# Kernel tuning notes

Hardware: AMD Instinct MI355X
Metric: run time of the kernel (lower is better)

Reference implementation:

```python
import jax, jax.numpy as jnp
import numpy as np

ALPHA = 0.2  # LeakyReLU negative slope
NEG_INF = -9e15


def setup_inputs() -> dict:
    key = jax.random.key(0)
    k1, k2, k3, k4 = jax.random.split(key, 4)
    B, N, Fin, Fout = 8, 2048, 512, 256
    x = jax.random.normal(k1, (B, N, Fin), dtype=jnp.float32)
    adj = jax.random.randint(k2, (B, N, N), 0, 2, dtype=jnp.int32)
    # xavier_uniform-like init, gain=1.414
    limW = 1.414 * np.sqrt(6.0 / (Fin + Fout))
    W = jax.random.uniform(k3, (Fin, Fout), jnp.float32, -limW, limW)
    lima = 1.414 * np.sqrt(6.0 / (2 * Fout + 1))
    a = jax.random.uniform(k4, (2 * Fout, 1), jnp.float32, -lima, lima)
    return {"x": x, "adj": adj, "W": W, "a": a}


def reference(x, adj, W, a):
    # x: [B,N,Fin], adj: [B,N,N], W: [Fin,Fout], a: [2*Fout,1]
    Fout = W.shape[1]
    h = jnp.einsum('bnf,fo->bno', x, W)                      # [B,N,Fout]
    a1 = a[:Fout, 0]                                         # source part
    a2 = a[Fout:, 0]                                         # target part
    # e_ij = LeakyReLU(a1.h_i + a2.h_j) -- decomposed, no O(N^2*2F) tensor
    s = h @ a1                                               # [B,N]
    t = h @ a2                                               # [B,N]
    e = jax.nn.leaky_relu(s[:, :, None] + t[:, None, :], ALPHA)  # [B,N,N]
    e = jnp.where(adj > 0, e, NEG_INF)
    attention = jax.nn.softmax(e, axis=2)                    # dropout p=0 (eval)
    h_prime = jnp.einsum('bij,bjo->bio', attention, h)       # [B,N,Fout]
    return jax.nn.elu(h_prime)                               # concat=True -> ELU
```

## Files before the change

kernel.cpp:

```cpp
#include <hip/hip_runtime.h>
#include <hip/hip_bf16.h>

typedef __attribute__((ext_vector_type(8))) short short8;
typedef __attribute__((ext_vector_type(4))) short short4v;
typedef __attribute__((ext_vector_type(4))) float f32x4;

constexpr int Bb = 8, NN = 2048, FIN = 512, FOUT = 256;
#define LRALPHA 0.2f
#define MFMA16(a, b, c) __builtin_amdgcn_mfma_f32_16x16x32_bf16((a), (b), (c), 0, 0, 0)

static __device__ __forceinline__ ushort f2bf(float f) {
    unsigned u = __float_as_uint(f);
    u += 0x7fffu + ((u >> 16) & 1u);
    return (ushort)(u >> 16);
}
static __device__ __forceinline__ float bf2f(ushort b) { return __uint_as_float(((unsigned)b) << 16); }

#define LDSBAR() do { asm volatile("s_waitcnt lgkmcnt(0)" ::: "memory"); \
                      __builtin_amdgcn_s_barrier(); \
                      asm volatile("" ::: "memory"); } while (0)
#define BARONLY() do { asm volatile("" ::: "memory"); \
                       __builtin_amdgcn_s_barrier(); \
                       asm volatile("" ::: "memory"); } while (0)

__global__ __launch_bounds__(256) void prep(const float* __restrict__ W,
                                            const float* __restrict__ a,
                                            ushort* __restrict__ WTh,
                                            ushort* __restrict__ WTl,
                                            float* __restrict__ wa1,
                                            float* __restrict__ wa2) {
    __shared__ float r1[4], r2[4];
    const int k = blockIdx.x, n = threadIdx.x;
    const int lane = n & 63, wv = n >> 6;
    const float w = W[(size_t)k * FOUT + n];
    const ushort hi = f2bf(w);
    WTh[(size_t)n * FIN + k] = hi;
    WTl[(size_t)n * FIN + k] = f2bf(w - bf2f(hi));
    float p1 = w * a[n], p2 = w * a[FOUT + n];
#pragma unroll
    for (int m = 1; m < 64; m <<= 1) {
        p1 += __shfl_xor(p1, m);
        p2 += __shfl_xor(p2, m);
    }
    if (lane == 0) { r1[wv] = p1; r2[wv] = p2; }
    __syncthreads();
    if (n == 0) {
        wa1[k] = r1[0] + r1[1] + r1[2] + r1[3];
        wa2[k] = r2[0] + r2[1] + r2[2] + r2[3];
    }
}

__global__ __launch_bounds__(512, 4) void gemm_h(const float* __restrict__ x,
                                                 const ushort* __restrict__ WTh,
                                                 const ushort* __restrict__ WTl,
                                                 const float* __restrict__ wa1,
                                                 const float* __restrict__ wa2,
                                                 ushort* __restrict__ hTh,
                                                 float* __restrict__ sv,
                                                 float* __restrict__ tv) {
    __shared__ ushort Ah[4][2][512];
    __shared__ ushort Tr[8][16][72];

    const int t = threadIdx.x, lane = t & 63, w = t >> 6;
    const int m0 = (blockIdx.x >> 1) * 64;
    const int n0 = (blockIdx.x & 1) * 128;

    const int lr = t >> 3, c8 = (t & 7) * 8;
    const int aif = lr >> 4, akstep = c8 >> 5, ak8 = (c8 >> 3) & 3;
    ushort* adst = &Ah[aif][akstep][(((ak8 << 4) | (lr & 15))) * 8];
    const float* xp = x + (size_t)(m0 + lr) * FIN + c8;

    const size_t boff = (size_t)(n0 + w * 16 + (lane & 15)) * FIN + (lane >> 4) * 8;
    const ushort* bph = WTh + boff;
    const ushort* bpl = WTl + boff;

    f32x4 acc[4];
#pragma unroll
    for (int f = 0; f < 4; ++f) acc[f] = (f32x4){0.f, 0.f, 0.f, 0.f};
    float sp = 0.f, tp = 0.f;

    float4 xa0 = *(const float4*)(xp + 0),  xa1 = *(const float4*)(xp + 4);
    float4 xb0 = *(const float4*)(xp + 64), xb1 = *(const float4*)(xp + 68);
    float4 xc0, xc1, xd0, xd1;
    short8 bhA0 = *(const short8*)(bph + 0),  blA0 = *(const short8*)(bpl + 0);
    short8 bhA1 = *(const short8*)(bph + 32), blA1 = *(const short8*)(bpl + 32);
    short8 bhB0, blB0, bhB1, blB1;

    auto phase = [&](int kt, const float4& c0, const float4& c1, float4& nx0, float4& nx1,
                     const short8& cbh0, const short8& cbl0, const short8& cbh1, const short8& cbl1,
                     short8& nbh0, short8& nbl0, short8& nbh1, short8& nbl1) {
        const int k0 = kt * 64;
        const float fv[8] = {c0.x, c0.y, c0.z, c0.w, c1.x, c1.y, c1.z, c1.w};
        short8 vh;
#pragma unroll
        for (int e = 0; e < 8; ++e) vh[e] = (short)f2bf(fv[e]);
        const float4 w1a = *(const float4*)(wa1 + k0 + c8);
        const float4 w1b = *(const float4*)(wa1 + k0 + c8 + 4);
        const float4 w2a = *(const float4*)(wa2 + k0 + c8);
        const float4 w2b = *(const float4*)(wa2 + k0 + c8 + 4);
        sp += fv[0]*w1a.x + fv[1]*w1a.y + fv[2]*w1a.z + fv[3]*w1a.w
            + fv[4]*w1b.x + fv[5]*w1b.y + fv[6]*w1b.z + fv[7]*w1b.w;
        tp += fv[0]*w2a.x + fv[1]*w2a.y + fv[2]*w2a.z + fv[3]*w2a.w
            + fv[4]*w2b.x + fv[5]*w2b.y + fv[6]*w2b.z + fv[7]*w2b.w;
        BARONLY();
        *(short8*)adst = vh;
        LDSBAR();
        const int kx = (kt + 2 < 8 ? kt + 2 : 7) * 64;
        nx0 = *(const float4*)(xp + kx);
        nx1 = *(const float4*)(xp + kx + 4);
        const int kb = (kt + 1 < 8 ? kt + 1 : 7) * 64;
        nbh0 = *(const short8*)(bph + kb);
        nbl0 = *(const short8*)(bpl + kb);
        nbh1 = *(const short8*)(bph + kb + 32);
        nbl1 = *(const short8*)(bpl + kb + 32);
#pragma unroll
        for (int f = 0; f < 4; ++f) {
            const short8 a0 = *(const short8*)&Ah[f][0][lane * 8];
            const short8 a1 = *(const short8*)&Ah[f][1][lane * 8];
            acc[f] = MFMA16(a0, cbh0, acc[f]);
            acc[f] = MFMA16(a0, cbl0, acc[f]);
            acc[f] = MFMA16(a1, cbh1, acc[f]);
            acc[f] = MFMA16(a1, cbl1, acc[f]);
        }
    };

    for (int kt = 0; kt < 8; kt += 4) {
        phase(kt + 0, xa0, xa1, xc0, xc1, bhA0, blA0, bhA1, blA1, bhB0, blB0, bhB1, blB1);
        phase(kt + 1, xb0, xb1, xd0, xd1, bhB0, blB0, bhB1, blB1, bhA0, blA0, bhA1, blA1);
        phase(kt + 2, xc0, xc1, xa0, xa1, bhA0, blA0, bhA1, blA1, bhB0, blB0, bhB1, blB1);
        phase(kt + 3, xd0, xd1, xb0, xb1, bhB0, blB0, bhB1, blB1, bhA0, blA0, bhA1, blA1);
    }

    sp += __shfl_xor(sp, 1, 8); sp += __shfl_xor(sp, 2, 8); sp += __shfl_xor(sp, 4, 8);
    tp += __shfl_xor(tp, 1, 8); tp += __shfl_xor(tp, 2, 8); tp += __shfl_xor(tp, 4, 8);
    if ((t & 7) == 0 && n0 == 0) {
        sv[m0 + lr] = sp;
        tv[m0 + lr] = tp;
    }

    const int rb = (lane >> 4) * 4;
#pragma unroll
    for (int f = 0; f < 4; ++f)
#pragma unroll
        for (int r = 0; r < 4; ++r)
            Tr[w][lane & 15][f * 16 + rb + r] = f2bf(acc[f][r]);
    __syncthreads();
    const int c = lane >> 2, rowb = (lane & 3) * 16;
    const ushort* src = &Tr[w][c][rowb];
    const short8 v0 = *(const short8*)src;
    const short8 v1 = *(const short8*)(src + 8);
    ushort* dst = hTh + ((size_t)(m0 >> 11) * FOUT + n0 + w * 16 + c) * NN + (m0 & 2047) + rowb;
    *(short8*)dst = v0;
    *(short8*)(dst + 8) = v1;
}

__global__ __launch_bounds__(512, 2) void gat_fused(const int* __restrict__ adj,
                                                    const ushort* __restrict__ hTh,
                                                    const float* __restrict__ sv,
                                                    const float* __restrict__ tv,
                                                    float* __restrict__ out) {
    __shared__ float t_l[NN];
    __shared__ ushort Pf[2][4][2][512];
    __shared__ float den_l[64];

    const int t = threadIdx.x, lane = t & 63, w = t >> 6;
    const int b = blockIdx.x & 7, i0 = (blockIdx.x >> 3) * 64;

    *(float4*)&t_l[t * 4] = *(const float4*)&tv[b * NN + t * 4];

    const int r = t >> 3, jn = (t & 7) * 8;
    const float s_i = sv[b * NN + i0 + r];
    const int* adjp = adj + ((size_t)b * NN + i0 + r) * NN + jn;
    const int pif = r >> 4, pkstep = jn >> 5, pk8 = (jn >> 3) & 3;
    ushort* pdst0 = &Pf[0][pif][pkstep][((pk8 << 4) | (r & 15)) * 8];
    ushort* pdst1 = &Pf[1][pif][pkstep][((pk8 << 4) | (r & 15)) * 8];

    const ushort* hb = hTh + (size_t)b * FOUT * NN;
    const ushort* h00 = hb + (size_t)(2 * w * 16 + (lane & 15)) * NN + (lane >> 4) * 8;
    const ushort* h10 = hb + (size_t)((2 * w + 1) * 16 + (lane & 15)) * NN + (lane >> 4) * 8;

    f32x4 acc[4][2];
#pragma unroll
    for (int f = 0; f < 4; ++f) {
        acc[f][0] = (f32x4){0.f, 0.f, 0.f, 0.f};
        acc[f][1] = (f32x4){0.f, 0.f, 0.f, 0.f};
    }
    float den_part = 0.f;

    int4 ajA0 = *(const int4*)(adjp),      ajA1 = *(const int4*)(adjp + 4);
    int4 ajB0 = *(const int4*)(adjp + 64), ajB1 = *(const int4*)(adjp + 68);
    int4 ajC0, ajC1, ajD0, ajD1;
    short8 X00 = *(const short8*)h00, X01 = *(const short8*)(h00 + 32);
    short8 X10 = *(const short8*)h10, X11 = *(const short8*)(h10 + 32);
    short8 Y00, Y01, Y10, Y11;

    __syncthreads();

    auto phase = [&](int jt, ushort* pdst, int rbuf,
                     const int4& ac0, const int4& ac1, int4& an0, int4& an1,
                     const short8& c00, const short8& c01, const short8& c10, const short8& c11,
                     short8& n00, short8& n01, short8& n10, short8& n11) {
        const int j0 = jt * 64;
        const int jH = min(j0 + 64, NN - 64);
        const int jA = min(j0 + 128, NN - 64);
        n00 = *(const short8*)(h00 + jH);
        n01 = *(const short8*)(h00 + jH + 32);
        n10 = *(const short8*)(h10 + jH);
        n11 = *(const short8*)(h10 + jH + 32);
        an0 = *(const int4*)(adjp + jA);
        an1 = *(const int4*)(adjp + jA + 4);
        const float4 tq0 = *(const float4*)&t_l[j0 + jn];
        const float4 tq1 = *(const float4*)&t_l[j0 + jn + 4];
        const float tvv[8] = {tq0.x, tq0.y, tq0.z, tq0.w, tq1.x, tq1.y, tq1.z, tq1.w};
        const int avs[8] = {ac0.x, ac0.y, ac0.z, ac0.w, ac1.x, ac1.y, ac1.z, ac1.w};
        short8 pv;
#pragma unroll
        for (int e = 0; e < 8; ++e) {
            float v = s_i + tvv[e];
            v = v > 0.f ? v : LRALPHA * v;
            const float wv = avs[e] > 0 ? __expf(v) : 0.f;
            const ushort hbv = f2bf(wv);
            den_part += bf2f(hbv);
            pv[e] = (short)hbv;
        }
        *(short8*)pdst = pv;
        LDSBAR();
        const ushort* pr = &Pf[rbuf][0][0][0] + lane * 8;
        __builtin_amdgcn_s_setprio(1);
#pragma unroll
        for (int f = 0; f < 4; ++f) {
            const short8 a0 = *(const short8*)(pr + f * 1024);
            const short8 a1 = *(const short8*)(pr + f * 1024 + 512);
            acc[f][0] = MFMA16(a0, c00, acc[f][0]);
            acc[f][0] = MFMA16(a1, c01, acc[f][0]);
            acc[f][1] = MFMA16(a0, c10, acc[f][1]);
            acc[f][1] = MFMA16(a1, c11, acc[f][1]);
        }
        __builtin_amdgcn_s_setprio(0);
    };

    for (int tt = 0; tt < NN / 64; tt += 4) {
        phase(tt + 0, pdst0, 0, ajA0, ajA1, ajC0, ajC1, X00, X01, X10, X11, Y00, Y01, Y10, Y11);
        phase(tt + 1, pdst1, 1, ajB0, ajB1, ajD0, ajD1, Y00, Y01, Y10, Y11, X00, X01, X10, X11);
        phase(tt + 2, pdst0, 0, ajC0, ajC1, ajA0, ajA1, X00, X01, X10, X11, Y00, Y01, Y10, Y11);
        phase(tt + 3, pdst1, 1, ajD0, ajD1, ajB0, ajB1, Y00, Y01, Y10, Y11, X00, X01, X10, X11);
    }

    den_part += __shfl_xor(den_part, 1, 8);
    den_part += __shfl_xor(den_part, 2, 8);
    den_part += __shfl_xor(den_part, 4, 8);
    if ((t & 7) == 0) den_l[r] = den_part;
    __syncthreads();

    const int rb = (lane >> 4) * 4;
#pragma unroll
    for (int f = 0; f < 4; ++f) {
#pragma unroll
        for (int rr = 0; rr < 4; ++rr) {
            const int row = f * 16 + rb + rr;
            const float inv = 1.0f / den_l[row];
#pragma unroll
            for (int cf = 0; cf < 2; ++cf) {
                float v = acc[f][cf][rr] * inv;
                v = v > 0.f ? v : expm1f(v);
                out[((size_t)b * NN + i0 + row) * FOUT + w * 32 + cf * 16 + (lane & 15)] = v;
            }
        }
    }
}

extern "C" void kernel_launch(void* const* d_in, const int* in_sizes, int n_in,
                              void* d_out, int out_size, void* d_ws, size_t ws_size,
                              hipStream_t stream) {
    const float* x   = (const float*)d_in[0];
    const int*   adj = (const int*)d_in[1];
    const float* W   = (const float*)d_in[2];
    const float* a   = (const float*)d_in[3];
    float* out = (float*)d_out;

    ushort* hTh = (ushort*)d_ws;
    float*  sv  = (float*)(hTh + (size_t)Bb * FOUT * NN);
    float*  tv  = sv + Bb * NN;
    ushort* WTh = (ushort*)(tv + Bb * NN);
    ushort* WTl = WTh + (size_t)FIN * FOUT;
    float*  wa1 = (float*)(WTl + (size_t)FIN * FOUT);
    float*  wa2 = wa1 + FIN;

    prep<<<FIN, 256, 0, stream>>>(W, a, WTh, WTl, wa1, wa2);
    gemm_h<<<512, 512, 0, stream>>>(x, WTh, WTl, wa1, wa2, hTh, sv, tv);
    gat_fused<<<256, 512, 0, stream>>>(adj, hTh, sv, tv, out);
}
```

Measured before the change: 270.5 us.

## Widen gemm_h tile to full output width and deepen adj prefetch in gat_fused

gemm_h now has each block compute all 256 output columns for 64 rows, with each wave owning two 16-column slices. This halves the grid and removes the duplicated x loads, bf16 conversion and s/t dot products that the two column-half blocks used to repeat, at the cost of more registers and lower occupancy. In gat_fused, adjacency loads are now issued four tiles ahead instead of two, and h loads are moved to after the MFMAs, to hide global latency for the int32 adj stream.

```diff
diff --git a/kernel.cpp b/kernel.cpp
--- a/kernel.cpp
+++ b/kernel.cpp
@@ -2,7 +2,6 @@
 #include <hip/hip_bf16.h>
 
 typedef __attribute__((ext_vector_type(8))) short short8;
-typedef __attribute__((ext_vector_type(4))) short short4v;
 typedef __attribute__((ext_vector_type(4))) float f32x4;
 
 constexpr int Bb = 8, NN = 2048, FIN = 512, FOUT = 256;
@@ -50,7 +49,7 @@
     }
 }
 
-__global__ __launch_bounds__(512, 4) void gemm_h(const float* __restrict__ x,
+__global__ __launch_bounds__(512, 2) void gemm_h(const float* __restrict__ x,
                                                  const ushort* __restrict__ WTh,
                                                  const ushort* __restrict__ WTl,
                                                  const float* __restrict__ wa1,
@@ -62,33 +61,40 @@
     __shared__ ushort Tr[8][16][72];
 
     const int t = threadIdx.x, lane = t & 63, w = t >> 6;
-    const int m0 = (blockIdx.x >> 1) * 64;
-    const int n0 = (blockIdx.x & 1) * 128;
+    const int m0 = blockIdx.x * 64;
 
     const int lr = t >> 3, c8 = (t & 7) * 8;
     const int aif = lr >> 4, akstep = c8 >> 5, ak8 = (c8 >> 3) & 3;
     ushort* adst = &Ah[aif][akstep][(((ak8 << 4) | (lr & 15))) * 8];
     const float* xp = x + (size_t)(m0 + lr) * FIN + c8;
 
-    const size_t boff = (size_t)(n0 + w * 16 + (lane & 15)) * FIN + (lane >> 4) * 8;
-    const ushort* bph = WTh + boff;
-    const ushort* bpl = WTl + boff;
-
-    f32x4 acc[4];
-#pragma unroll
-    for (int f = 0; f < 4; ++f) acc[f] = (f32x4){0.f, 0.f, 0.f, 0.f};
+    const size_t b0 = (size_t)(w * 32 + (lane & 15)) * FIN + (lane >> 4) * 8;
+    const size_t b1 = b0 + (size_t)16 * FIN;
+    const ushort *ph0 = WTh + b0, *pl0 = WTl + b0;
+    const ushort *ph1 = WTh + b1, *pl1 = WTl + b1;
+
+    f32x4 acc[4][2];
+#pragma unroll
+    for (int f = 0; f < 4; ++f) {
+        acc[f][0] = (f32x4){0.f, 0.f, 0.f, 0.f};
+        acc[f][1] = (f32x4){0.f, 0.f, 0.f, 0.f};
+    }
     float sp = 0.f, tp = 0.f;
 
     float4 xa0 = *(const float4*)(xp + 0),  xa1 = *(const float4*)(xp + 4);
     float4 xb0 = *(const float4*)(xp + 64), xb1 = *(const float4*)(xp + 68);
     float4 xc0, xc1, xd0, xd1;
-    short8 bhA0 = *(const short8*)(bph + 0),  blA0 = *(const short8*)(bpl + 0);
-    short8 bhA1 = *(const short8*)(bph + 32), blA1 = *(const short8*)(bpl + 32);
-    short8 bhB0, blB0, bhB1, blB1;
+    short8 A00 = *(const short8*)(ph0 + 0),  A01 = *(const short8*)(pl0 + 0);
+    short8 A02 = *(const short8*)(ph0 + 32), A03 = *(const short8*)(pl0 + 32);
+    short8 A10 = *(const short8*)(ph1 + 0),  A11 = *(const short8*)(pl1 + 0);
+    short8 A12 = *(const short8*)(ph1 + 32), A13 = *(const short8*)(pl1 + 32);
+    short8 B00, B01, B02, B03, B10, B11, B12, B13;
 
     auto phase = [&](int kt, const float4& c0, const float4& c1, float4& nx0, float4& nx1,
-                     const short8& cbh0, const short8& cbl0, const short8& cbh1, const short8& cbl1,
-                     short8& nbh0, short8& nbl0, short8& nbh1, short8& nbl1) {
+                     const short8& g00, const short8& g01, const short8& g02, const short8& g03,
+                     const short8& g10, const short8& g11, const short8& g12, const short8& g13,
+                     short8& n00, short8& n01, short8& n02, short8& n03,
+                     short8& n10, short8& n11, short8& n12, short8& n13) {
         const int k0 = kt * 64;
         const float fv[8] = {c0.x, c0.y, c0.z, c0.w, c1.x, c1.y, c1.z, c1.w};
         short8 vh;
@@ -109,49 +115,62 @@
         nx0 = *(const float4*)(xp + kx);
         nx1 = *(const float4*)(xp + kx + 4);
         const int kb = (kt + 1 < 8 ? kt + 1 : 7) * 64;
-        nbh0 = *(const short8*)(bph + kb);
-        nbl0 = *(const short8*)(bpl + kb);
-        nbh1 = *(const short8*)(bph + kb + 32);
-        nbl1 = *(const short8*)(bpl + kb + 32);
+        n00 = *(const short8*)(ph0 + kb);      n01 = *(const short8*)(pl0 + kb);
+        n02 = *(const short8*)(ph0 + kb + 32); n03 = *(const short8*)(pl0 + kb + 32);
+        n10 = *(const short8*)(ph1 + kb);      n11 = *(const short8*)(pl1 + kb);
+        n12 = *(const short8*)(ph1 + kb + 32); n13 = *(const short8*)(pl1 + kb + 32);
 #pragma unroll
         for (int f = 0; f < 4; ++f) {
             const short8 a0 = *(const short8*)&Ah[f][0][lane * 8];
             const short8 a1 = *(const short8*)&Ah[f][1][lane * 8];
-            acc[f] = MFMA16(a0, cbh0, acc[f]);
-            acc[f] = MFMA16(a0, cbl0, acc[f]);
-            acc[f] = MFMA16(a1, cbh1, acc[f]);
-            acc[f] = MFMA16(a1, cbl1, acc[f]);
+            acc[f][0] = MFMA16(a0, g00, acc[f][0]);
+            acc[f][0] = MFMA16(a0, g01, acc[f][0]);
+            acc[f][0] = MFMA16(a1, g02, acc[f][0]);
+            acc[f][0] = MFMA16(a1, g03, acc[f][0]);
+            acc[f][1] = MFMA16(a0, g10, acc[f][1]);
+            acc[f][1] = MFMA16(a0, g11, acc[f][1]);
+            acc[f][1] = MFMA16(a1, g12, acc[f][1]);
+            acc[f][1] = MFMA16(a1, g13, acc[f][1]);
         }
     };
 
     for (int kt = 0; kt < 8; kt += 4) {
-        phase(kt + 0, xa0, xa1, xc0, xc1, bhA0, blA0, bhA1, blA1, bhB0, blB0, bhB1, blB1);
-        phase(kt + 1, xb0, xb1, xd0, xd1, bhB0, blB0, bhB1, blB1, bhA0, blA0, bhA1, blA1);
-        phase(kt + 2, xc0, xc1, xa0, xa1, bhA0, blA0, bhA1, blA1, bhB0, blB0, bhB1, blB1);
-        phase(kt + 3, xd0, xd1, xb0, xb1, bhB0, blB0, bhB1, blB1, bhA0, blA0, bhA1, blA1);
+        phase(kt + 0, xa0, xa1, xc0, xc1, A00,A01,A02,A03,A10,A11,A12,A13,
+                                           B00,B01,B02,B03,B10,B11,B12,B13);
+        phase(kt + 1, xb0, xb1, xd0, xd1, B00,B01,B02,B03,B10,B11,B12,B13,
+                                           A00,A01,A02,A03,A10,A11,A12,A13);
+        phase(kt + 2, xc0, xc1, xa0, xa1, A00,A01,A02,A03,A10,A11,A12,A13,
+                                           B00,B01,B02,B03,B10,B11,B12,B13);
+        phase(kt + 3, xd0, xd1, xb0, xb1, B00,B01,B02,B03,B10,B11,B12,B13,
+                                           A00,A01,A02,A03,A10,A11,A12,A13);
     }
 
     sp += __shfl_xor(sp, 1, 8); sp += __shfl_xor(sp, 2, 8); sp += __shfl_xor(sp, 4, 8);
     tp += __shfl_xor(tp, 1, 8); tp += __shfl_xor(tp, 2, 8); tp += __shfl_xor(tp, 4, 8);
-    if ((t & 7) == 0 && n0 == 0) {
+    if ((t & 7) == 0) {
         sv[m0 + lr] = sp;
         tv[m0 + lr] = tp;
     }
 
     const int rb = (lane >> 4) * 4;
-#pragma unroll
-    for (int f = 0; f < 4; ++f)
-#pragma unroll
-        for (int r = 0; r < 4; ++r)
-            Tr[w][lane & 15][f * 16 + rb + r] = f2bf(acc[f][r]);
-    __syncthreads();
     const int c = lane >> 2, rowb = (lane & 3) * 16;
-    const ushort* src = &Tr[w][c][rowb];
-    const short8 v0 = *(const short8*)src;
-    const short8 v1 = *(const short8*)(src + 8);
-    ushort* dst = hTh + ((size_t)(m0 >> 11) * FOUT + n0 + w * 16 + c) * NN + (m0 & 2047) + rowb;
-    *(short8*)dst = v0;
-    *(short8*)(dst + 8) = v1;
+#pragma unroll
+    for (int p = 0; p < 2; ++p) {
+        __syncthreads();
+#pragma unroll
+        for (int f = 0; f < 4; ++f)
+#pragma unroll
+            for (int r = 0; r < 4; ++r)
+                Tr[w][lane & 15][f * 16 + rb + r] = f2bf(acc[f][p][r]);
+        __syncthreads();
+        const ushort* src = &Tr[w][c][rowb];
+        const short8 v0 = *(const short8*)src;
+        const short8 v1 = *(const short8*)(src + 8);
+        ushort* dst = hTh + ((size_t)(m0 >> 11) * FOUT + w * 32 + p * 16 + c) * NN
+                      + (m0 & 2047) + rowb;
+        *(short8*)dst = v0;
+        *(short8*)(dst + 8) = v1;
+    }
 }
 
 __global__ __launch_bounds__(512, 2) void gat_fused(const int* __restrict__ adj,
@@ -187,32 +206,28 @@
     }
     float den_part = 0.f;
 
-    int4 ajA0 = *(const int4*)(adjp),      ajA1 = *(const int4*)(adjp + 4);
-    int4 ajB0 = *(const int4*)(adjp + 64), ajB1 = *(const int4*)(adjp + 68);
-    int4 ajC0, ajC1, ajD0, ajD1;
-    short8 X00 = *(const short8*)h00, X01 = *(const short8*)(h00 + 32);
-    short8 X10 = *(const short8*)h10, X11 = *(const short8*)(h10 + 32);
-    short8 Y00, Y01, Y10, Y11;
+    int4 ajA0 = *(const int4*)(adjp +   0), ajA1 = *(const int4*)(adjp +   4);
+    int4 ajB0 = *(const int4*)(adjp +  64), ajB1 = *(const int4*)(adjp +  68);
+    int4 ajC0 = *(const int4*)(adjp + 128), ajC1 = *(const int4*)(adjp + 132);
+    int4 ajD0 = *(const int4*)(adjp + 192), ajD1 = *(const int4*)(adjp + 196);
+    short8 X00 = *(const short8*)h00,        X01 = *(const short8*)(h00 + 32);
+    short8 X10 = *(const short8*)h10,        X11 = *(const short8*)(h10 + 32);
+    short8 Y00 = *(const short8*)(h00 + 64), Y01 = *(const short8*)(h00 + 96);
+    short8 Y10 = *(const short8*)(h10 + 64), Y11 = *(const short8*)(h10 + 96);
 
     __syncthreads();
 
     auto phase = [&](int jt, ushort* pdst, int rbuf,
-                     const int4& ac0, const int4& ac1, int4& an0, int4& an1,
-                     const short8& c00, const short8& c01, const short8& c10, const short8& c11,
-                     short8& n00, short8& n01, short8& n10, short8& n11) {
+                     int4& as0, int4& as1,
+                     short8& H00, short8& H01, short8& H10, short8& H11) {
         const int j0 = jt * 64;
-        const int jH = min(j0 + 64, NN - 64);
-        const int jA = min(j0 + 128, NN - 64);
-        n00 = *(const short8*)(h00 + jH);
-        n01 = *(const short8*)(h00 + jH + 32);
-        n10 = *(const short8*)(h10 + jH);
-        n11 = *(const short8*)(h10 + jH + 32);
-        an0 = *(const int4*)(adjp + jA);
-        an1 = *(const int4*)(adjp + jA + 4);
+        const int avs[8] = {as0.x, as0.y, as0.z, as0.w, as1.x, as1.y, as1.z, as1.w};
+        const int jA = min(j0 + 256, NN - 64);
+        as0 = *(const int4*)(adjp + jA);
+        as1 = *(const int4*)(adjp + jA + 4);
         const float4 tq0 = *(const float4*)&t_l[j0 + jn];
         const float4 tq1 = *(const float4*)&t_l[j0 + jn + 4];
         const float tvv[8] = {tq0.x, tq0.y, tq0.z, tq0.w, tq1.x, tq1.y, tq1.z, tq1.w};
-        const int avs[8] = {ac0.x, ac0.y, ac0.z, ac0.w, ac1.x, ac1.y, ac1.z, ac1.w};
         short8 pv;
 #pragma unroll
         for (int e = 0; e < 8; ++e) {
@@ -231,19 +246,24 @@
         for (int f = 0; f < 4; ++f) {
             const short8 a0 = *(const short8*)(pr + f * 1024);
             const short8 a1 = *(const short8*)(pr + f * 1024 + 512);
-            acc[f][0] = MFMA16(a0, c00, acc[f][0]);
-            acc[f][0] = MFMA16(a1, c01, acc[f][0]);
-            acc[f][1] = MFMA16(a0, c10, acc[f][1]);
-            acc[f][1] = MFMA16(a1, c11, acc[f][1]);
+            acc[f][0] = MFMA16(a0, H00, acc[f][0]);
+            acc[f][0] = MFMA16(a1, H01, acc[f][0]);
+            acc[f][1] = MFMA16(a0, H10, acc[f][1]);
+            acc[f][1] = MFMA16(a1, H11, acc[f][1]);
         }
         __builtin_amdgcn_s_setprio(0);
+        const int jH = min(j0 + 128, NN - 64);
+        H00 = *(const short8*)(h00 + jH);
+        H01 = *(const short8*)(h00 + jH + 32);
+        H10 = *(const short8*)(h10 + jH);
+        H11 = *(const short8*)(h10 + jH + 32);
     };
 
     for (int tt = 0; tt < NN / 64; tt += 4) {
-        phase(tt + 0, pdst0, 0, ajA0, ajA1, ajC0, ajC1, X00, X01, X10, X11, Y00, Y01, Y10, Y11);
-        phase(tt + 1, pdst1, 1, ajB0, ajB1, ajD0, ajD1, Y00, Y01, Y10, Y11, X00, X01, X10, X11);
-        phase(tt + 2, pdst0, 0, ajC0, ajC1, ajA0, ajA1, X00, X01, X10, X11, Y00, Y01, Y10, Y11);
-        phase(tt + 3, pdst1, 1, ajD0, ajD1, ajB0, ajB1, Y00, Y01, Y10, Y11, X00, X01, X10, X11);
+        phase(tt + 0, pdst0, 0, ajA0, ajA1, X00, X01, X10, X11);
+        phase(tt + 1, pdst1, 1, ajB0, ajB1, Y00, Y01, Y10, Y11);
+        phase(tt + 2, pdst0, 0, ajC0, ajC1, X00, X01, X10, X11);
+        phase(tt + 3, pdst1, 1, ajD0, ajD1, Y00, Y01, Y10, Y11);
     }
 
     den_part += __shfl_xor(den_part, 1, 8);
@@ -287,6 +307,6 @@
     float*  wa2 = wa1 + FIN;
 
     prep<<<FIN, 256, 0, stream>>>(W, a, WTh, WTl, wa1, wa2);
-    gemm_h<<<512, 512, 0, stream>>>(x, WTh, WTl, wa1, wa2, hTh, sv, tv);
+    gemm_h<<<256, 512, 0, stream>>>(x, WTh, WTl, wa1, wa2, hTh, sv, tv);
     gat_fused<<<256, 512, 0, stream>>>(adj, hTh, sv, tv, out);
 }
```

Result: faster. 261.9 us (-3.2%).
